# Kernel tuning notes

Hardware: AMD Instinct MI355X
Metric: run time of the kernel (lower is better)

Reference implementation:

```python
import jax, jax.numpy as jnp
import numpy as np

B, S, D, H, E, K = 4, 2048, 1024, 2048, 8, 2


def setup_inputs() -> dict:
    key = jax.random.key(0)
    ks = jax.random.split(key, 6)
    s_d = 1.0 / np.sqrt(D)
    s_h = 1.0 / np.sqrt(H)
    return {
        "x": jax.random.normal(ks[0], (B, S, D), dtype=jnp.float32),
        "Wg": jax.random.normal(ks[1], (D, E), dtype=jnp.float32) * s_d,
        "bg": jnp.zeros((E,), dtype=jnp.float32),
        "w1": jax.random.normal(ks[2], (E, D, H), dtype=jnp.float32) * s_d,
        "w3": jax.random.normal(ks[3], (E, D, H), dtype=jnp.float32) * s_d,
        "w2": jax.random.normal(ks[4], (E, H, D), dtype=jnp.float32) * s_h,
    }


def reference(x, Wg, bg, w1, w3, w2):
    # Router (eval mode: no noise). logits: [B,S,E]
    logits = jnp.einsum("bsd,de->bse", x, Wg) + bg
    top_v, top_i = jax.lax.top_k(logits, K)          # [B,S,K]
    probs = jax.nn.softmax(top_v, axis=-1)           # softmax over -inf-masked logits == softmax over top-k
    # Scatter top-k probs back to dense gates [B,S,E] (zeros elsewhere)
    gates = jnp.sum(jax.nn.one_hot(top_i, E, dtype=x.dtype) * probs[..., None], axis=-2)
    # Combine: gate-weighted sum of per-expert SwiGLU FFN outputs.
    # gates[...,e] == 0 exactly for tokens not routed to expert e, matching the
    # original masked gather -> FFN -> weighted scatter-add.
    out = jnp.zeros_like(x)
    for e in range(E):
        h = jax.nn.silu(x @ w1[e]) * (x @ w3[e])     # [B,S,H]
        y = h @ w2[e]                                # [B,S,D]
        out = out + gates[..., e:e + 1] * y
    return out
```

## Files before the change

kernel.cpp:

```cpp
#include <hip/hip_runtime.h>

typedef short bf16x8 __attribute__((ext_vector_type(8)));
typedef float f32x4 __attribute__((ext_vector_type(4)));
typedef unsigned short u16;
typedef unsigned int u32;

#define TOKS 8192
#define DDIM 1024
#define HDIM 2048
#define NEXP 8
#define ROWS_TOTAL (2 * TOKS)

#define WL1_CAP 544
#define WL2_CAP 136

#define NSUB 32
#define SUBCAP 256
#define CSTRIDE 32

__device__ __forceinline__ u16 f2b(float f) {
  u32 x;
  __builtin_memcpy(&x, &f, 4);
  return (u16)((x + 0x7fffu + ((x >> 16) & 1u)) >> 16);
}

typedef const __attribute__((address_space(1))) u32* gp_t;
typedef __attribute__((address_space(3))) u32* lp_t;
__device__ __forceinline__ void glds16(const void* g, void* l) {
  __builtin_amdgcn_global_load_lds((gp_t)g, (lp_t)l, 16, 0, 0);
}

__global__ __launch_bounds__(256) void cvt_x_kernel(const float* __restrict__ in,
                                                    u16* __restrict__ out) {
  size_t i = ((size_t)blockIdx.x * 256 + threadIdx.x) * 8;
  float4 a = *(const float4*)(in + i);
  float4 b = *(const float4*)(in + i + 4);
  union { int4 v; u16 u[8]; } o;
  o.u[0] = f2b(a.x); o.u[1] = f2b(a.y); o.u[2] = f2b(a.z); o.u[3] = f2b(a.w);
  o.u[4] = f2b(b.x); o.u[5] = f2b(b.y); o.u[6] = f2b(b.z); o.u[7] = f2b(b.w);
  *(int4*)(out + i) = o.v;
}

__global__ __launch_bounds__(256) void cvt_wT_kernel(const float* __restrict__ in,
                                                     u16* __restrict__ out, int K, int N) {
  size_t eo = (size_t)blockIdx.z * K * N;
  in += eo; out += eo;
  int n0 = blockIdx.x * 64, k0 = blockIdx.y * 64;
  __shared__ u16 s[64][72];
  int tid = threadIdx.x;
  int kr = tid >> 4, nc = (tid & 15) * 4;
#pragma unroll
  for (int i = 0; i < 4; ++i) {
    int k = k0 + i * 16 + kr;
    float4 v = *(const float4*)(in + (size_t)k * N + n0 + nc);
    ushort4 u;
    u.x = f2b(v.x); u.y = f2b(v.y); u.z = f2b(v.z); u.w = f2b(v.w);
    *(ushort4*)&s[i * 16 + kr][nc] = u;
  }
  __syncthreads();
  int nl = tid >> 2, kc = tid & 3;
  union { int4 v[2]; u16 u[16]; } o;
#pragma unroll
  for (int j = 0; j < 16; ++j) o.u[j] = s[kc * 16 + j][nl];
  u16* op = out + (size_t)(n0 + nl) * K + k0 + kc * 16;
  *(int4*)op = o.v[0];
  *(int4*)(op + 8) = o.v[1];
}

__global__ __launch_bounds__(256) void cvt_wc_kernel(const float* __restrict__ in,
                                                     u16* __restrict__ out, int K, int N,
                                                     int half) {
  in += (size_t)blockIdx.z * K * N;
  out += (size_t)blockIdx.z * 2 * K * N;
  int n0 = blockIdx.x * 64, k0 = blockIdx.y * 64;
  __shared__ u16 s[64][72];
  int tid = threadIdx.x;
  int kr = tid >> 4, nc = (tid & 15) * 4;
#pragma unroll
  for (int i = 0; i < 4; ++i) {
    int k = k0 + i * 16 + kr;
    float4 v = *(const float4*)(in + (size_t)k * N + n0 + nc);
    ushort4 u;
    u.x = f2b(v.x); u.y = f2b(v.y); u.z = f2b(v.z); u.w = f2b(v.w);
    *(ushort4*)&s[i * 16 + kr][nc] = u;
  }
  __syncthreads();
  int nl = tid >> 2, kc = tid & 3;
  union { int4 v[2]; u16 u[16]; } o;
#pragma unroll
  for (int j = 0; j < 16; ++j) o.u[j] = s[kc * 16 + j][nl];
  int n = n0 + nl;
  int orow = ((n >> 4) << 5) + half * 16 + (n & 15);
  u16* op = out + (size_t)orow * K + k0 + kc * 16;
  *(int4*)op = o.v[0];
  *(int4*)(op + 8) = o.v[1];
}

__global__ __launch_bounds__(256) void router_kernel(
    const float* __restrict__ x, const float* __restrict__ Wg,
    const float* __restrict__ bg, int* __restrict__ counts32,
    int* __restrict__ tok16, float* __restrict__ g16) {
  int lane = threadIdx.x & 63;
  int t = blockIdx.x * 4 + (threadIdx.x >> 6);
  int sub = blockIdx.x & (NSUB - 1);
  const float* xr = x + (size_t)t * DDIM;
  float acc[NEXP];
#pragma unroll
  for (int e = 0; e < NEXP; ++e) acc[e] = 0.f;
#pragma unroll
  for (int jj = 0; jj < DDIM / 64; ++jj) {
    int d = jj * 64 + lane;
    float xv = xr[d];
    float4 w0 = *(const float4*)(Wg + d * NEXP);
    float4 w1v = *(const float4*)(Wg + d * NEXP + 4);
    acc[0] += xv * w0.x; acc[1] += xv * w0.y; acc[2] += xv * w0.z; acc[3] += xv * w0.w;
    acc[4] += xv * w1v.x; acc[5] += xv * w1v.y; acc[6] += xv * w1v.z; acc[7] += xv * w1v.w;
  }
#pragma unroll
  for (int off = 32; off > 0; off >>= 1) {
#pragma unroll
    for (int e = 0; e < NEXP; ++e) acc[e] += __shfl_down(acc[e], off, 64);
  }
  if (lane == 0) {
    float v[NEXP];
#pragma unroll
    for (int e = 0; e < NEXP; ++e) v[e] = acc[e] + bg[e];
    int e0 = 0;
    float v0 = v[0];
#pragma unroll
    for (int e = 1; e < NEXP; ++e)
      if (v[e] > v0) { v0 = v[e]; e0 = e; }
    int e1 = -1;
    float v1 = -3.4e38f;
#pragma unroll
    for (int e = 0; e < NEXP; ++e)
      if (e != e0 && v[e] > v1) { v1 = v[e]; e1 = e; }
    if (e1 < 0) e1 = (e0 + 1) & 7;
    float ex = __expf(v1 - v0);
    float g0 = 1.f / (1.f + ex);
    float g1 = 1.f - g0;
    int c0 = sub * NEXP + e0;
    int s0 = atomicAdd(&counts32[c0 * CSTRIDE], 1);
    if (s0 < SUBCAP) { tok16[c0 * SUBCAP + s0] = t; g16[c0 * SUBCAP + s0] = g0; }
    int c1 = sub * NEXP + e1;
    int s1 = atomicAdd(&counts32[c1 * CSTRIDE], 1);
    if (s1 < SUBCAP) { tok16[c1 * SUBCAP + s1] = t; g16[c1 * SUBCAP + s1] = g1; }
  }
}

__global__ void offsets_kernel(const int* __restrict__ counts32, int* __restrict__ counts,
                               int* __restrict__ offsets, int* __restrict__ dstbase,
                               int* __restrict__ wl1, int* __restrict__ wl2) {
  if (threadIdx.x == 0) {
    for (int e = 0; e < NEXP; ++e) {
      int run = 0;
      for (int sub = 0; sub < NSUB; ++sub) {
        int idx = sub * NEXP + e;
        dstbase[idx] = run;
        run += counts32[idx * CSTRIDE];
      }
      counts[e] = run;
    }
    int o = 0;
    for (int e = 0; e < NEXP; ++e) { offsets[e] = o; o += counts[e]; }
    int j1 = 0, j2 = 0;
    for (int e = 0; e < NEXP; ++e) {
      int me = (counts[e] + 127) >> 7;
      for (int m = 0; m < me; ++m) {
        if (j1 + 4 <= WL1_CAP) {
#pragma unroll
          for (int yq = 0; yq < 4; ++yq) wl1[1 + j1 + yq] = (e << 8) | (m << 2) | yq;
          j1 += 4;
        }
        if (j2 < WL2_CAP) wl2[1 + j2++] = (e << 8) | m;
      }
    }
    wl1[0] = j1; wl2[0] = j2;
  }
}

__global__ __launch_bounds__(256) void compact_kernel(
    const int* __restrict__ counts32, const int* __restrict__ dstbase,
    const int* __restrict__ tok16, const float* __restrict__ g16,
    int* __restrict__ tok_ids, float* __restrict__ gates) {
  int idx = blockIdx.x;
  int e = idx & (NEXP - 1);
  int n = counts32[idx * CSTRIDE];
  if (n > SUBCAP) n = SUBCAP;
  int base = dstbase[idx];
  for (int i = threadIdx.x; i < n; i += 256) {
    tok_ids[e * TOKS + base + i] = tok16[idx * SUBCAP + i];
    gates[e * TOKS + base + i]   = g16[idx * SUBCAP + i];
  }
}

__global__ __launch_bounds__(256, 3) void ffn1_kernel(
    const u16* __restrict__ xb, const u16* __restrict__ wc,
    const int* __restrict__ tok_ids, const int* __restrict__ counts,
    const int* __restrict__ offsets, const int* __restrict__ wl,
    u16* __restrict__ h, int nbase_wc, int hw, int e_arg) {
  int e, m, y;
  if (e_arg >= 0) {
    e = e_arg; m = blockIdx.x; y = blockIdx.y;
    if (m * 128 >= counts[e]) return;
  } else {
    int bid = blockIdx.x;
    int xcd = bid & 7, j = bid >> 3;
    if (j >= wl[0]) return;
    int w = wl[1 + j];
    e = w >> 8; m = (w >> 2) & 63; y = xcd * 4 + (w & 3);
  }
  int count = counts[e];
  int mbase = m * 128;
  int row_off = (e_arg >= 0) ? 0 : offsets[e];
  int n0w = nbase_wc + y * 128;
  size_t we = (e_arg >= 0) ? 0 : (size_t)e;
  const u16* wce = wc + we * (size_t)(2 * HDIM * DDIM);

  __shared__ u16 sA[128 * 64];
  __shared__ u16 sB[128 * 64];
  __shared__ int stok[128];

  int tid = threadIdx.x, lane = tid & 63, wv = tid >> 6;
  if (tid < 128) {
    int s = mbase + tid;
    if (s >= count) s = count - 1;
    stok[tid] = tok_ids[e * TOKS + s];
  }
  __syncthreads();

  int rloc = lane >> 3, ch = lane & 7;
  u32 offA[4], offB[4];
#pragma unroll
  for (int i = 0; i < 4; ++i) {
    int r = (wv * 4 + i) * 8 + rloc;
    int sw = ch ^ (r & 7);
    offA[i] = (u32)stok[r] * DDIM + sw * 8;
    offB[i] = (u32)(n0w + r) * DDIM + sw * 8;
  }

  int wm = wv >> 1, wn = wv & 1;
  int rsel = lane & 15, q = lane >> 4;

  f32x4 acc[4][4];
#pragma unroll
  for (int i = 0; i < 4; ++i)
#pragma unroll
    for (int j = 0; j < 4; ++j) {
      f32x4 z = {0.f, 0.f, 0.f, 0.f};
      acc[i][j] = z;
    }

  for (int k0 = 0; k0 < DDIM; k0 += 64) {
    __syncthreads();
#pragma unroll
    for (int i = 0; i < 4; ++i) {
      int sbase = (wv * 4 + i) * 512;
      glds16(xb  + offA[i] + k0, sA + sbase);
      glds16(wce + offB[i] + k0, sB + sbase);
    }
    __syncthreads();

#pragma unroll
    for (int ks = 0; ks < 2; ++ks) {
      bf16x8 aF[4], bF[4];
#pragma unroll
      for (int mi = 0; mi < 4; ++mi) {
        int r = wm * 64 + mi * 16 + rsel;
        int p = (ks * 4 + q) ^ (r & 7);
        aF[mi] = *(const bf16x8*)&sA[r * 64 + p * 8];
      }
#pragma unroll
      for (int ni = 0; ni < 4; ++ni) {
        int r = wn * 64 + ni * 16 + rsel;
        int p = (ks * 4 + q) ^ (r & 7);
        bF[ni] = *(const bf16x8*)&sB[r * 64 + p * 8];
      }
#pragma unroll
      for (int mi = 0; mi < 4; ++mi)
#pragma unroll
        for (int ni = 0; ni < 4; ++ni)
          acc[mi][ni] = __builtin_amdgcn_mfma_f32_16x16x32_bf16(aF[mi], bF[ni], acc[mi][ni], 0, 0, 0);
    }
  }

  int cm = count - mbase;
#pragma unroll
  for (int mi = 0; mi < 4; ++mi) {
#pragma unroll
    for (int rr = 0; rr < 4; ++rr) {
      int mrow = wm * 64 + mi * 16 + q * 4 + rr;
      if (mrow < cm) {
#pragma unroll
        for (int np = 0; np < 2; ++np) {
          int hcol = y * 64 + (wn * 2 + np) * 16 + rsel;
          float u = acc[mi][2 * np][rr];
          float vv = acc[mi][2 * np + 1][rr];
          float hv = (u / (1.f + __expf(-u))) * vv;
          h[(size_t)(row_off + mbase + mrow) * hw + hcol] = f2b(hv);
        }
      }
    }
  }
}

__global__ __launch_bounds__(256) void ffn2_kernel(
    const u16* __restrict__ h, const u16* __restrict__ w2t,
    const int* __restrict__ tok_ids, const float* __restrict__ gates,
    const int* __restrict__ counts, const int* __restrict__ offsets,
    const int* __restrict__ wl, float* __restrict__ out, int kbase, int hw, int e_arg) {
  int e, m, y;
  if (e_arg >= 0) {
    e = e_arg; m = blockIdx.x; y = blockIdx.y;
    if (m * 128 >= counts[e]) return;
  } else {
    int bid = blockIdx.x;
    int xcd = bid & 7, j = bid >> 3;
    if (j >= wl[0]) return;
    int w = wl[1 + j];
    e = w >> 8; m = w & 63; y = xcd;
  }
  int count = counts[e];
  int mbase = m * 128;
  int row_off = (e_arg >= 0) ? 0 : offsets[e];
  int n0 = y * 128;
  size_t we = (e_arg >= 0) ? 0 : (size_t)e;
  const u16* w2e = w2t + we * (size_t)(HDIM * DDIM);

  __shared__ u16 sA[128 * 64];
  __shared__ u16 sB[128 * 64];
  __shared__ int stok[128];
  __shared__ float sg[128];

  int tid = threadIdx.x, lane = tid & 63, wv = tid >> 6;
  if (tid < 128) {
    int s = mbase + tid;
    if (s >= count) s = count - 1;
    stok[tid] = tok_ids[e * TOKS + s];
    sg[tid] = gates[e * TOKS + s];
  }
  __syncthreads();

  int rloc = lane >> 3, ch = lane & 7;
  u32 offA[4], offB[4];
#pragma unroll
  for (int i = 0; i < 4; ++i) {
    int r = (wv * 4 + i) * 8 + rloc;
    int sw = ch ^ (r & 7);
    int slot = mbase + r;
    if (slot >= count) slot = count - 1;
    offA[i] = (u32)(row_off + slot) * hw + sw * 8;
    offB[i] = (u32)(n0 + r) * HDIM + kbase + sw * 8;
  }

  int wm = wv >> 1, wn = wv & 1;
  int rsel = lane & 15, q = lane >> 4;

  f32x4 acc[4][4];
#pragma unroll
  for (int i = 0; i < 4; ++i)
#pragma unroll
    for (int j = 0; j < 4; ++j) {
      f32x4 z = {0.f, 0.f, 0.f, 0.f};
      acc[i][j] = z;
    }

  for (int k0 = 0; k0 < hw; k0 += 64) {
    __syncthreads();
#pragma unroll
    for (int i = 0; i < 4; ++i) {
      int sbase = (wv * 4 + i) * 512;
      glds16(h   + offA[i] + k0, sA + sbase);
      glds16(w2e + offB[i] + k0, sB + sbase);
    }
    __syncthreads();

#pragma unroll
    for (int ks = 0; ks < 2; ++ks) {
      bf16x8 aF[4], bF[4];
#pragma unroll
      for (int mi = 0; mi < 4; ++mi) {
        int r = wm * 64 + mi * 16 + rsel;
        int p = (ks * 4 + q) ^ (r & 7);
        aF[mi] = *(const bf16x8*)&sA[r * 64 + p * 8];
      }
#pragma unroll
      for (int ni = 0; ni < 4; ++ni) {
        int r = wn * 64 + ni * 16 + rsel;
        int p = (ks * 4 + q) ^ (r & 7);
        bF[ni] = *(const bf16x8*)&sB[r * 64 + p * 8];
      }
#pragma unroll
      for (int mi = 0; mi < 4; ++mi)
#pragma unroll
        for (int ni = 0; ni < 4; ++ni)
          acc[mi][ni] = __builtin_amdgcn_mfma_f32_16x16x32_bf16(aF[mi], bF[ni], acc[mi][ni], 0, 0, 0);
    }
  }

  int cm = count - mbase;
#pragma unroll
  for (int mi = 0; mi < 4; ++mi) {
#pragma unroll
    for (int rr = 0; rr < 4; ++rr) {
      int mrow = wm * 64 + mi * 16 + q * 4 + rr;
      if (mrow < cm) {
        int t = stok[mrow];
        float g = sg[mrow];
#pragma unroll
        for (int ni = 0; ni < 4; ++ni) {
          int col = n0 + wn * 64 + ni * 16 + rsel;
          atomicAdd(&out[(size_t)t * DDIM + col], g * acc[mi][ni][rr]);
        }
      }
    }
  }
}

extern "C" void kernel_launch(void* const* d_in, const int* in_sizes, int n_in,
                              void* d_out, int out_size, void* d_ws, size_t ws_size,
                              hipStream_t stream) {
  (void)in_sizes; (void)n_in; (void)out_size;
  const float* x  = (const float*)d_in[0];
  const float* Wg = (const float*)d_in[1];
  const float* bg = (const float*)d_in[2];
  const float* w1 = (const float*)d_in[3];
  const float* w3 = (const float*)d_in[4];
  const float* w2 = (const float*)d_in[5];
  float* out = (float*)d_out;

  char* ws = (char*)d_ws;
  int*   tok_ids  = (int*)ws;
  float* gates    = (float*)(ws + 262144);
  int*   counts   = (int*)(ws + 524288);
  int*   offsets  = (int*)(ws + 524352);
  int*   wl1      = (int*)(ws + 524416);
  int*   wl2      = (int*)(ws + 528512);
  int*   dstbase  = (int*)(ws + 529536);
  int*   counts32 = (int*)(ws + 532480);
  int*   tok16    = (int*)(ws + 565248);
  float* g16      = (float*)(ws + 827392);
  u16*   xb       = (u16*)(ws + (2 << 20));

  const size_t WEXP  = (size_t)HDIM * DDIM * 2;
  const size_t WALL  = 3ull * NEXP * WEXP;
  const size_t HFULL = (size_t)ROWS_TOTAL * HDIM * 2;
  const size_t base  = (2 << 20) + 16777216ull;

  hipMemsetAsync(counts32, 0, NEXP * NSUB * CSTRIDE * 4, stream);
  hipMemsetAsync(out, 0, (size_t)TOKS * DDIM * 4, stream);

  cvt_x_kernel<<<TOKS * DDIM / (256 * 8), 256, 0, stream>>>(x, xb);
  router_kernel<<<TOKS / 4, 256, 0, stream>>>(x, Wg, bg, counts32, tok16, g16);
  offsets_kernel<<<1, 64, 0, stream>>>(counts32, counts, offsets, dstbase, wl1, wl2);
  compact_kernel<<<NSUB * NEXP, 256, 0, stream>>>(counts32, dstbase, tok16, g16,
                                                  tok_ids, gates);

  if (ws_size >= base + WALL + HFULL) {
    u16* wcb = (u16*)(ws + base);
    u16* w2t = wcb + (size_t)NEXP * 2 * HDIM * DDIM;
    u16* hb  = w2t + (size_t)NEXP * HDIM * DDIM;
    cvt_wc_kernel<<<dim3(HDIM / 64, DDIM / 64, NEXP), 256, 0, stream>>>(w1, wcb, DDIM, HDIM, 0);
    cvt_wc_kernel<<<dim3(HDIM / 64, DDIM / 64, NEXP), 256, 0, stream>>>(w3, wcb, DDIM, HDIM, 1);
    cvt_wT_kernel<<<dim3(DDIM / 64, HDIM / 64, NEXP), 256, 0, stream>>>(w2, w2t, HDIM, DDIM);
    ffn1_kernel<<<dim3(8 * WL1_CAP), 256, 0, stream>>>(
        xb, wcb, tok_ids, counts, offsets, wl1, hb, 0, HDIM, -1);
    ffn2_kernel<<<dim3(8 * WL2_CAP), 256, 0, stream>>>(
        hb, w2t, tok_ids, gates, counts, offsets, wl2, out, 0, HDIM, -1);
  } else {
    int hw = 128;
    const int cand[5] = {2048, 1024, 512, 256, 128};
    for (int i = 0; i < 5; ++i)
      if (base + 3 * WEXP + (size_t)TOKS * cand[i] * 2 <= ws_size) { hw = cand[i]; break; }
    u16* wcb = (u16*)(ws + base);
    u16* w2t = wcb + (size_t)2 * HDIM * DDIM;
    u16* hb  = w2t + (size_t)HDIM * DDIM;
    for (int e = 0; e < NEXP; ++e) {
      cvt_wc_kernel<<<dim3(HDIM / 64, DDIM / 64, 1), 256, 0, stream>>>(
          w1 + (size_t)e * DDIM * HDIM, wcb, DDIM, HDIM, 0);
      cvt_wc_kernel<<<dim3(HDIM / 64, DDIM / 64, 1), 256, 0, stream>>>(
          w3 + (size_t)e * DDIM * HDIM, wcb, DDIM, HDIM, 1);
      cvt_wT_kernel<<<dim3(DDIM / 64, HDIM / 64, 1), 256, 0, stream>>>(
          w2 + (size_t)e * HDIM * DDIM, w2t, HDIM, DDIM);
      for (int nb = 0; nb < HDIM; nb += hw) {
        ffn1_kernel<<<dim3(64, hw / 64, 1), 256, 0, stream>>>(
            xb, wcb, tok_ids, counts, offsets, nullptr, hb, 2 * nb, hw, e);
        ffn2_kernel<<<dim3(64, DDIM / 128, 1), 256, 0, stream>>>(
            hb, w2t, tok_ids, gates, counts, offsets, nullptr, out, nb, hw, e);
      }
    }
  }
}
```

Measured before the change: 579.5 us.

## Double-buffer LDS tiles in FFN GEMMs and parallelize offset scan

```diff
diff --git a/kernel.cpp b/kernel.cpp
--- a/kernel.cpp
+++ b/kernel.cpp
@@ -151,21 +151,25 @@
 __global__ void offsets_kernel(const int* __restrict__ counts32, int* __restrict__ counts,
                                int* __restrict__ offsets, int* __restrict__ dstbase,
                                int* __restrict__ wl1, int* __restrict__ wl2) {
-  if (threadIdx.x == 0) {
-    for (int e = 0; e < NEXP; ++e) {
-      int run = 0;
-      for (int sub = 0; sub < NSUB; ++sub) {
-        int idx = sub * NEXP + e;
-        dstbase[idx] = run;
-        run += counts32[idx * CSTRIDE];
-      }
-      counts[e] = run;
-    }
+  int t = threadIdx.x;
+  __shared__ int sc[NEXP];
+  if (t < NEXP) {
+    int c[NSUB];
+#pragma unroll
+    for (int sub = 0; sub < NSUB; ++sub) c[sub] = counts32[(sub * NEXP + t) * CSTRIDE];
+    int run = 0;
+#pragma unroll
+    for (int sub = 0; sub < NSUB; ++sub) { dstbase[sub * NEXP + t] = run; run += c[sub]; }
+    counts[t] = run;
+    sc[t] = run;
+  }
+  __syncthreads();
+  if (t == 0) {
     int o = 0;
-    for (int e = 0; e < NEXP; ++e) { offsets[e] = o; o += counts[e]; }
+    for (int e = 0; e < NEXP; ++e) { offsets[e] = o; o += sc[e]; }
     int j1 = 0, j2 = 0;
     for (int e = 0; e < NEXP; ++e) {
-      int me = (counts[e] + 127) >> 7;
+      int me = (sc[e] + 127) >> 7;
       for (int m = 0; m < me; ++m) {
         if (j1 + 4 <= WL1_CAP) {
 #pragma unroll
@@ -194,7 +198,7 @@
   }
 }
 
-__global__ __launch_bounds__(256, 3) void ffn1_kernel(
+__global__ __launch_bounds__(256, 2) void ffn1_kernel(
     const u16* __restrict__ xb, const u16* __restrict__ wc,
     const int* __restrict__ tok_ids, const int* __restrict__ counts,
     const int* __restrict__ offsets, const int* __restrict__ wl,
@@ -217,8 +221,8 @@
   size_t we = (e_arg >= 0) ? 0 : (size_t)e;
   const u16* wce = wc + we * (size_t)(2 * HDIM * DDIM);
 
-  __shared__ u16 sA[128 * 64];
-  __shared__ u16 sB[128 * 64];
+  __shared__ u16 sA[2][128 * 64];
+  __shared__ u16 sB[2][128 * 64];
   __shared__ int stok[128];
 
   int tid = threadIdx.x, lane = tid & 63, wv = tid >> 6;
@@ -231,12 +235,14 @@
 
   int rloc = lane >> 3, ch = lane & 7;
   u32 offA[4], offB[4];
+  int sbase[4];
 #pragma unroll
   for (int i = 0; i < 4; ++i) {
     int r = (wv * 4 + i) * 8 + rloc;
     int sw = ch ^ (r & 7);
     offA[i] = (u32)stok[r] * DDIM + sw * 8;
     offB[i] = (u32)(n0w + r) * DDIM + sw * 8;
+    sbase[i] = (wv * 4 + i) * 512;
   }
 
   int wm = wv >> 1, wn = wv & 1;
@@ -251,16 +257,29 @@
       acc[i][j] = z;
     }
 
-  for (int k0 = 0; k0 < DDIM; k0 += 64) {
-    __syncthreads();
-#pragma unroll
-    for (int i = 0; i < 4; ++i) {
-      int sbase = (wv * 4 + i) * 512;
-      glds16(xb  + offA[i] + k0, sA + sbase);
-      glds16(wce + offB[i] + k0, sB + sbase);
-    }
-    __syncthreads();
-
+#pragma unroll
+  for (int i = 0; i < 4; ++i) {
+    glds16(xb  + offA[i], &sA[0][sbase[i]]);
+    glds16(wce + offB[i], &sB[0][sbase[i]]);
+  }
+
+  const int NKT = DDIM / 64;
+  for (int kt = 0; kt < NKT; ++kt) {
+    int cur = kt & 1;
+    if (kt + 1 < NKT) {
+      int kn = (kt + 1) * 64;
+#pragma unroll
+      for (int i = 0; i < 4; ++i) {
+        glds16(xb  + offA[i] + kn, &sA[cur ^ 1][sbase[i]]);
+        glds16(wce + offB[i] + kn, &sB[cur ^ 1][sbase[i]]);
+      }
+      asm volatile("s_waitcnt vmcnt(8)" ::: "memory");
+    } else {
+      asm volatile("s_waitcnt vmcnt(0)" ::: "memory");
+    }
+    __builtin_amdgcn_s_barrier();
+
+    __builtin_amdgcn_s_setprio(1);
 #pragma unroll
     for (int ks = 0; ks < 2; ++ks) {
       bf16x8 aF[4], bF[4];
@@ -268,13 +287,13 @@
       for (int mi = 0; mi < 4; ++mi) {
         int r = wm * 64 + mi * 16 + rsel;
         int p = (ks * 4 + q) ^ (r & 7);
-        aF[mi] = *(const bf16x8*)&sA[r * 64 + p * 8];
+        aF[mi] = *(const bf16x8*)&sA[cur][r * 64 + p * 8];
       }
 #pragma unroll
       for (int ni = 0; ni < 4; ++ni) {
         int r = wn * 64 + ni * 16 + rsel;
         int p = (ks * 4 + q) ^ (r & 7);
-        bF[ni] = *(const bf16x8*)&sB[r * 64 + p * 8];
+        bF[ni] = *(const bf16x8*)&sB[cur][r * 64 + p * 8];
       }
 #pragma unroll
       for (int mi = 0; mi < 4; ++mi)
@@ -282,6 +301,8 @@
         for (int ni = 0; ni < 4; ++ni)
           acc[mi][ni] = __builtin_amdgcn_mfma_f32_16x16x32_bf16(aF[mi], bF[ni], acc[mi][ni], 0, 0, 0);
     }
+    __builtin_amdgcn_s_setprio(0);
+    __builtin_amdgcn_s_barrier();
   }
 
   int cm = count - mbase;
@@ -304,7 +325,7 @@
   }
 }
 
-__global__ __launch_bounds__(256) void ffn2_kernel(
+__global__ __launch_bounds__(256, 2) void ffn2_kernel(
     const u16* __restrict__ h, const u16* __restrict__ w2t,
     const int* __restrict__ tok_ids, const float* __restrict__ gates,
     const int* __restrict__ counts, const int* __restrict__ offsets,
@@ -327,8 +348,8 @@
   size_t we = (e_arg >= 0) ? 0 : (size_t)e;
   const u16* w2e = w2t + we * (size_t)(HDIM * DDIM);
 
-  __shared__ u16 sA[128 * 64];
-  __shared__ u16 sB[128 * 64];
+  __shared__ u16 sA[2][128 * 64];
+  __shared__ u16 sB[2][128 * 64];
   __shared__ int stok[128];
   __shared__ float sg[128];
 
@@ -343,6 +364,7 @@
 
   int rloc = lane >> 3, ch = lane & 7;
   u32 offA[4], offB[4];
+  int sbase[4];
 #pragma unroll
   for (int i = 0; i < 4; ++i) {
     int r = (wv * 4 + i) * 8 + rloc;
@@ -351,6 +373,7 @@
     if (slot >= count) slot = count - 1;
     offA[i] = (u32)(row_off + slot) * hw + sw * 8;
     offB[i] = (u32)(n0 + r) * HDIM + kbase + sw * 8;
+    sbase[i] = (wv * 4 + i) * 512;
   }
 
   int wm = wv >> 1, wn = wv & 1;
@@ -365,16 +388,29 @@
       acc[i][j] = z;
     }
 
-  for (int k0 = 0; k0 < hw; k0 += 64) {
-    __syncthreads();
-#pragma unroll
-    for (int i = 0; i < 4; ++i) {
-      int sbase = (wv * 4 + i) * 512;
-      glds16(h   + offA[i] + k0, sA + sbase);
-      glds16(w2e + offB[i] + k0, sB + sbase);
-    }
-    __syncthreads();
-
+#pragma unroll
+  for (int i = 0; i < 4; ++i) {
+    glds16(h   + offA[i], &sA[0][sbase[i]]);
+    glds16(w2e + offB[i], &sB[0][sbase[i]]);
+  }
+
+  const int NKT2 = hw / 64;
+  for (int kt = 0; kt < NKT2; ++kt) {
+    int cur = kt & 1;
+    if (kt + 1 < NKT2) {
+      int kn = (kt + 1) * 64;
+#pragma unroll
+      for (int i = 0; i < 4; ++i) {
+        glds16(h   + offA[i] + kn, &sA[cur ^ 1][sbase[i]]);
+        glds16(w2e + offB[i] + kn, &sB[cur ^ 1][sbase[i]]);
+      }
+      asm volatile("s_waitcnt vmcnt(8)" ::: "memory");
+    } else {
+      asm volatile("s_waitcnt vmcnt(0)" ::: "memory");
+    }
+    __builtin_amdgcn_s_barrier();
+
+    __builtin_amdgcn_s_setprio(1);
 #pragma unroll
     for (int ks = 0; ks < 2; ++ks) {
       bf16x8 aF[4], bF[4];
@@ -382,13 +418,13 @@
       for (int mi = 0; mi < 4; ++mi) {
         int r = wm * 64 + mi * 16 + rsel;
         int p = (ks * 4 + q) ^ (r & 7);
-        aF[mi] = *(const bf16x8*)&sA[r * 64 + p * 8];
+        aF[mi] = *(const bf16x8*)&sA[cur][r * 64 + p * 8];
       }
 #pragma unroll
       for (int ni = 0; ni < 4; ++ni) {
         int r = wn * 64 + ni * 16 + rsel;
         int p = (ks * 4 + q) ^ (r & 7);
-        bF[ni] = *(const bf16x8*)&sB[r * 64 + p * 8];
+        bF[ni] = *(const bf16x8*)&sB[cur][r * 64 + p * 8];
       }
 #pragma unroll
       for (int mi = 0; mi < 4; ++mi)
@@ -396,6 +432,8 @@
         for (int ni = 0; ni < 4; ++ni)
           acc[mi][ni] = __builtin_amdgcn_mfma_f32_16x16x32_bf16(aF[mi], bF[ni], acc[mi][ni], 0, 0, 0);
     }
+    __builtin_amdgcn_s_setprio(0);
+    __builtin_amdgcn_s_barrier();
   }
 
   int cm = count - mbase;
```

Result: slower. 641.6 us (+10.7%).
